# Kernel optimization log

Measured on AMD Instinct MI355X. Metric: run time of the kernel, lower is better.

Reference implementation:

```python
import jax, jax.numpy as jnp
import numpy as np

EPS = 1e-8

def rmsnorm(x, w):
    norm = jax.lax.rsqrt(jnp.mean(x * x, axis=-1, keepdims=True) + EPS)
    return x * norm * w

def setup_inputs() -> dict:
    key = jax.random.key(0)
    ks = jax.random.split(key, 10)
    B, L, D, S = 8, 4096, 1024, 256
    sD = 1.0 / np.sqrt(D)
    sS = 1.0 / np.sqrt(S)
    return {
        "x": jax.random.normal(ks[0], (B, L, D), jnp.float32),
        "w_norm": jnp.ones((D,), jnp.float32),
        "W_in": jax.random.normal(ks[1], (D, 3 * S), jnp.float32) * sD,
        "b_in": jnp.zeros((3 * S,), jnp.float32),
        "W_x": jax.random.normal(ks[2], (S, S), jnp.float32) * sS,
        "b_x": jnp.zeros((S,), jnp.float32),
        "W_dt": jax.random.normal(ks[3], (S, S), jnp.float32) * sS,
        "b_dt": jnp.zeros((S,), jnp.float32),
        "W_out": jax.random.normal(ks[4], (S, D), jnp.float32) * sS,
        "b_out": jnp.zeros((D,), jnp.float32),
    }

def reference(x, w_norm, W_in, b_in, W_x, b_x, W_dt, b_dt, W_out, b_out):
    # MambaLikeBlock forward (dropout=0 / eval mode)
    residual = x
    xn = rmsnorm(x, w_norm)
    uzg = xn @ W_in + b_in                       # [B,L,3S]
    S = uzg.shape[-1] // 3
    u, z, g = uzg[..., :S], uzg[..., S:2 * S], uzg[..., 2 * S:]
    # per-step projections are time-independent -> precompute for all t
    ut = jnp.tanh(u @ W_x + b_x)                 # [B,L,S]
    dt = jax.nn.sigmoid(z @ W_dt + b_dt)         # [B,L,S]

    def step(h, inp):
        u_t, dt_t = inp
        h = (1.0 - dt_t) * h + dt_t * u_t
        return h, h

    h0 = jnp.zeros(ut.shape[::2][::-1][:0] + (ut.shape[0], ut.shape[2]), ut.dtype)  # [B,S]
    _, hs = jax.lax.scan(step, h0, (ut.transpose(1, 0, 2), dt.transpose(1, 0, 2)))
    hs = hs.transpose(1, 0, 2)                   # [B,L,S]
    y = hs * jax.nn.sigmoid(g)
    y = y @ W_out + b_out                        # [B,L,D]
    return residual + y
```

## Files before the change

### kernel.cpp

```cpp
#include <hip/hip_runtime.h>
#include <hip/hip_bf16.h>

#define BB 8
#define LL 4096
#define DD 1024
#define SS 256
#define NTOK (BB * LL)
#define CCH 64
#define TCH (LL / CCH)

typedef short bf16x8 __attribute__((ext_vector_type(8)));
typedef float f32x4 __attribute__((ext_vector_type(4)));

__device__ __forceinline__ float bfu(unsigned short v) {
  union { unsigned int i; float f; } x;
  x.i = ((unsigned int)v) << 16;
  return x.f;
}

__device__ __forceinline__ void gl_lds16(const __hip_bfloat16* g, void* l) {
  __builtin_amdgcn_global_load_lds(
      (const __attribute__((address_space(1))) unsigned int*)g,
      (__attribute__((address_space(3))) unsigned int*)l, 16, 0, 0);
}

__global__ __launch_bounds__(256) void prep_rms(const float* __restrict__ x,
                                                const float* __restrict__ wn,
                                                __hip_bfloat16* __restrict__ xn) {
  const size_t row = blockIdx.x;
  const int t = threadIdx.x;
  const float4 xv = reinterpret_cast<const float4*>(x + row * DD)[t];
  const float4 wv = reinterpret_cast<const float4*>(wn)[t];
  float ss = xv.x * xv.x + xv.y * xv.y + xv.z * xv.z + xv.w * xv.w;
#pragma unroll
  for (int m = 32; m >= 1; m >>= 1) ss += __shfl_xor(ss, m);
  __shared__ float red[4];
  if ((t & 63) == 0) red[t >> 6] = ss;
  __syncthreads();
  const float tot = red[0] + red[1] + red[2] + red[3];
  const float r = rsqrtf(tot * (1.0f / DD) + 1e-8f);
  union { ushort4 u; __hip_bfloat16 h[4]; } o;
  o.h[0] = __float2bfloat16(xv.x * wv.x * r);
  o.h[1] = __float2bfloat16(xv.y * wv.y * r);
  o.h[2] = __float2bfloat16(xv.z * wv.z * r);
  o.h[3] = __float2bfloat16(xv.w * wv.w * r);
  reinterpret_cast<ushort4*>(xn + row * DD)[t] = o.u;
}

__global__ __launch_bounds__(256) void convT4(
    const float* __restrict__ W0, const float* __restrict__ W1,
    const float* __restrict__ W2, const float* __restrict__ W3,
    __hip_bfloat16* __restrict__ T0, __hip_bfloat16* __restrict__ T1,
    __hip_bfloat16* __restrict__ T2, __hip_bfloat16* __restrict__ T3) {
  const int seg = blockIdx.y;
  const int K = (seg == 0) ? DD : SS;
  const int Nw = (seg == 0) ? 768 : (seg == 3) ? DD : SS;
  const float* W = (seg == 0) ? W0 : (seg == 1) ? W1 : (seg == 2) ? W2 : W3;
  __hip_bfloat16* T = (seg == 0) ? T0 : (seg == 1) ? T1 : (seg == 2) ? T2 : T3;
  const int idx = blockIdx.x * 256 + threadIdx.x;
  if (idx >= K * Nw) return;
  const int k = idx / Nw, n = idx % Nw;
  T[(size_t)n * K + k] = __float2bfloat16(W[idx]);
}

template <int EPI>
__global__ __launch_bounds__(256, 2) void gemm_bf16(
    const __hip_bfloat16* __restrict__ A, int lda,
    const __hip_bfloat16* __restrict__ BT,
    const float* __restrict__ bias,
    void* __restrict__ Cptr, int ldc,
    const float* __restrict__ resid,
    int K) {
  __shared__ __align__(16) char ldsA[2][128 * 128];
  __shared__ __align__(16) char ldsB[2][128 * 128];

  const int t = threadIdx.x;
  const int bm = blockIdx.x, bn = blockIdx.y;
  const int wave = t >> 6, lane = t & 63;
  const int wr = (wave >> 1) * 64;
  const int wc = (wave & 1) * 64;
  const int lr = lane & 15;
  const int kg = lane >> 4;
  const int rsw = lr & 7;

  const int srow = lane >> 3;
  const int sg = (lane & 7) ^ srow;
  const int g_row = wave * 32 + srow;
  const __hip_bfloat16* Ab = A + (size_t)(bm * 128 + g_row) * lda + sg * 8;
  const __hip_bfloat16* Bb = BT + (size_t)(bn * 128 + g_row) * K + sg * 8;

  f32x4 acc[4][4] = {};

#define STAGE(d, koff)                                                        \
  {                                                                           \
    _Pragma("unroll") for (int p = 0; p < 4; ++p) {                           \
      gl_lds16(Ab + (size_t)(p * 8) * lda + (koff),                           \
               ldsA[d] + (wave * 32 + p * 8) * 128);                          \
      gl_lds16(Bb + (size_t)(p * 8) * K + (koff),                             \
               ldsB[d] + (wave * 32 + p * 8) * 128);                          \
    }                                                                         \
  }

  const int NT = K >> 6;
  STAGE(0, 0);

  for (int ti = 0; ti < NT; ++ti) {
    const int cur = ti & 1;
    if (ti + 1 < NT) {
      STAGE(cur ^ 1, (ti + 1) * 64);
      asm volatile("s_waitcnt vmcnt(8)" ::: "memory");
    } else {
      asm volatile("s_waitcnt vmcnt(0)" ::: "memory");
    }
    __builtin_amdgcn_sched_barrier(0);
    __builtin_amdgcn_s_barrier();
#pragma unroll
    for (int kh = 0; kh < 2; ++kh) {
      bf16x8 af[4], bfr[4];
#pragma unroll
      for (int m = 0; m < 4; ++m) {
        const int row = wr + m * 16 + lr;
        const int slot = (kg + kh * 4) ^ rsw;
        af[m] = *reinterpret_cast<const bf16x8*>(ldsA[cur] + row * 128 + slot * 16);
      }
#pragma unroll
      for (int n = 0; n < 4; ++n) {
        const int row = wc + n * 16 + lr;
        const int slot = (kg + kh * 4) ^ rsw;
        bfr[n] = *reinterpret_cast<const bf16x8*>(ldsB[cur] + row * 128 + slot * 16);
      }
#pragma unroll
      for (int m = 0; m < 4; ++m)
#pragma unroll
        for (int n = 0; n < 4; ++n)
          acc[m][n] = __builtin_amdgcn_mfma_f32_16x16x32_bf16(bfr[n], af[m],
                                                              acc[m][n], 0, 0, 0);
    }
    __builtin_amdgcn_sched_barrier(0);
    __builtin_amdgcn_s_barrier();
  }
#undef STAGE

  const int row0 = bm * 128 + wr + lr;
  const int col0 = bn * 128 + wc + kg * 4;
#pragma unroll
  for (int m = 0; m < 4; ++m) {
    const int row = row0 + m * 16;
#pragma unroll
    for (int n = 0; n < 4; ++n) {
      const int colb = col0 + n * 16;
      const float4 bv = *reinterpret_cast<const float4*>(&bias[colb]);
      float v0 = acc[m][n][0] + bv.x;
      float v1 = acc[m][n][1] + bv.y;
      float v2 = acc[m][n][2] + bv.z;
      float v3 = acc[m][n][3] + bv.w;
      if (EPI == 3) {
        const size_t off = (size_t)row * ldc + colb;
        const float4 rv = *reinterpret_cast<const float4*>(&resid[off]);
        float4 ov;
        ov.x = v0 + rv.x; ov.y = v1 + rv.y; ov.z = v2 + rv.z; ov.w = v3 + rv.w;
        *reinterpret_cast<float4*>(&((float*)Cptr)[off]) = ov;
      } else {
        if (EPI == 1) {
          v0 = tanhf(v0); v1 = tanhf(v1); v2 = tanhf(v2); v3 = tanhf(v3);
        } else if (EPI == 2) {
          v0 = 1.f / (1.f + expf(-v0)); v1 = 1.f / (1.f + expf(-v1));
          v2 = 1.f / (1.f + expf(-v2)); v3 = 1.f / (1.f + expf(-v3));
        }
        union { ushort4 u; __hip_bfloat16 h[4]; } o;
        o.h[0] = __float2bfloat16(v0); o.h[1] = __float2bfloat16(v1);
        o.h[2] = __float2bfloat16(v2); o.h[3] = __float2bfloat16(v3);
        *reinterpret_cast<ushort4*>(
            &((__hip_bfloat16*)Cptr)[(size_t)row * ldc + colb]) = o.u;
      }
    }
  }
}

__global__ __launch_bounds__(128) void scan_phase_a(
    const __hip_bfloat16* __restrict__ ut,
    const __hip_bfloat16* __restrict__ dtb,
    float* __restrict__ h0s, float* __restrict__ As) {
  const int bc = blockIdx.x;
  const int b = bc / CCH, c = bc % CCH;
  const int ch = threadIdx.x * 2;
  const size_t base = ((size_t)b * LL + (size_t)c * TCH) * SS + ch;
  float h0 = 0.f, h1 = 0.f, A0 = 1.f, A1 = 1.f;
#pragma unroll 8
  for (int t = 0; t < TCH; ++t) {
    const ushort2 uu = *reinterpret_cast<const ushort2*>(ut + base + (size_t)t * SS);
    const ushort2 dd = *reinterpret_cast<const ushort2*>(dtb + base + (size_t)t * SS);
    const float d0 = bfu(dd.x), d1 = bfu(dd.y);
    h0 = fmaf(d0, bfu(uu.x) - h0, h0);
    h1 = fmaf(d1, bfu(uu.y) - h1, h1);
    A0 *= (1.f - d0);
    A1 *= (1.f - d1);
  }
  const size_t o = (size_t)bc * SS + ch;
  *reinterpret_cast<float2*>(h0s + o) = make_float2(h0, h1);
  *reinterpret_cast<float2*>(As + o) = make_float2(A0, A1);
}

__global__ __launch_bounds__(256) void scan_phase_b(
    const float* __restrict__ h0s, const float* __restrict__ As,
    float* __restrict__ hins) {
  const int b = blockIdx.x;
  const int s = threadIdx.x;
  float hin = 0.f;
#pragma unroll 8
  for (int c = 0; c < CCH; ++c) {
    const size_t idx = ((size_t)b * CCH + c) * SS + s;
    hins[idx] = hin;
    hin = fmaf(As[idx], hin, h0s[idx]);
  }
}

__global__ __launch_bounds__(128) void scan_phase_c(
    const __hip_bfloat16* __restrict__ ut,
    const __hip_bfloat16* __restrict__ dtb,
    const __hip_bfloat16* __restrict__ gz,
    const float* __restrict__ hins,
    __hip_bfloat16* __restrict__ hsg) {
  const int bc = blockIdx.x;
  const int b = bc / CCH, c = bc % CCH;
  const int ch = threadIdx.x * 2;
  const size_t rowbase = (size_t)b * LL + (size_t)c * TCH;
  const float2 hv = *reinterpret_cast<const float2*>(hins + (size_t)bc * SS + ch);
  float h0 = hv.x, h1 = hv.y;
#pragma unroll 8
  for (int t = 0; t < TCH; ++t) {
    const size_t row = rowbase + t;
    const ushort2 uu = *reinterpret_cast<const ushort2*>(ut + row * SS + ch);
    const ushort2 dd = *reinterpret_cast<const ushort2*>(dtb + row * SS + ch);
    const ushort2 gg = *reinterpret_cast<const ushort2*>(gz + row * 768 + ch);
    h0 = fmaf(bfu(dd.x), bfu(uu.x) - h0, h0);
    h1 = fmaf(bfu(dd.y), bfu(uu.y) - h1, h1);
    union { ushort2 u; __hip_bfloat16 h[2]; } o;
    o.h[0] = __float2bfloat16(h0 / (1.f + expf(-bfu(gg.x))));
    o.h[1] = __float2bfloat16(h1 / (1.f + expf(-bfu(gg.y))));
    *reinterpret_cast<ushort2*>(hsg + row * SS + ch) = o.u;
  }
}

extern "C" void kernel_launch(void* const* d_in, const int* in_sizes, int n_in,
                              void* d_out, int out_size, void* d_ws, size_t ws_size,
                              hipStream_t stream) {
  const float* x      = (const float*)d_in[0];
  const float* w_norm = (const float*)d_in[1];
  const float* W_in   = (const float*)d_in[2];
  const float* b_in   = (const float*)d_in[3];
  const float* W_x    = (const float*)d_in[4];
  const float* b_x    = (const float*)d_in[5];
  const float* W_dt   = (const float*)d_in[6];
  const float* b_dt   = (const float*)d_in[7];
  const float* W_out  = (const float*)d_in[8];
  const float* b_out  = (const float*)d_in[9];
  float* out = (float*)d_out;

  char* w = (char*)d_ws;
  __hip_bfloat16* xn  = (__hip_bfloat16*)w;
  __hip_bfloat16* ut  = (__hip_bfloat16*)w;
  __hip_bfloat16* dtb = (__hip_bfloat16*)(w + (size_t)NTOK * SS * 2);
  w += (size_t)NTOK * DD * 2;
  __hip_bfloat16* uzg = (__hip_bfloat16*)w;  w += (size_t)NTOK * 768 * 2;
  __hip_bfloat16* WinT  = (__hip_bfloat16*)w;  w += (size_t)768 * DD * 2;
  __hip_bfloat16* WxT   = (__hip_bfloat16*)w;  w += (size_t)SS * SS * 2;
  __hip_bfloat16* WdtT  = (__hip_bfloat16*)w;  w += (size_t)SS * SS * 2;
  __hip_bfloat16* WoutT = (__hip_bfloat16*)w;  w += (size_t)DD * SS * 2;
  float* h0s  = (float*)w;  w += (size_t)BB * CCH * SS * 4;
  float* As   = (float*)w;  w += (size_t)BB * CCH * SS * 4;
  float* hins = (float*)w;  w += (size_t)BB * CCH * SS * 4;
  (void)ws_size; (void)n_in; (void)in_sizes; (void)out_size;

  convT4<<<dim3((DD * 768 + 255) / 256, 4), 256, 0, stream>>>(
      W_in, W_x, W_dt, W_out, WinT, WxT, WdtT, WoutT);

  prep_rms<<<NTOK, 256, 0, stream>>>(x, w_norm, xn);

  gemm_bf16<0><<<dim3(NTOK / 128, 768 / 128), 256, 0, stream>>>(
      xn, DD, WinT, b_in, uzg, 768, nullptr, DD);

  gemm_bf16<1><<<dim3(NTOK / 128, SS / 128), 256, 0, stream>>>(
      uzg, 768, WxT, b_x, ut, SS, nullptr, SS);
  gemm_bf16<2><<<dim3(NTOK / 128, SS / 128), 256, 0, stream>>>(
      uzg + SS, 768, WdtT, b_dt, dtb, SS, nullptr, SS);

  scan_phase_a<<<BB * CCH, 128, 0, stream>>>(ut, dtb, h0s, As);
  scan_phase_b<<<BB, 256, 0, stream>>>(h0s, As, hins);
  scan_phase_c<<<BB * CCH, 128, 0, stream>>>(ut, dtb, uzg + 2 * SS, hins, ut);

  gemm_bf16<3><<<dim3(NTOK / 128, DD / 128), 256, 0, stream>>>(
      ut, SS, WoutT, b_out, out, DD, x, SS);
}
```

Measured before the change: 276.9 us.

## Add LDS-free direct-load GEMM for K=256 projections and output GEMM

Adds a gemm_k256 kernel for the K=256 GEMMs (W_x, W_dt, W_out). It loads A and B fragments straight from global memory into registers for the MFMAs, with no LDS staging or barriers. The output GEMM gives each block two 128-column tiles so the A rows are reused across them. The old generic GEMM epilogue is reduced to a plain bf16 store, since only EPI 0 still uses it. The cost removed is LDS traffic and barrier sync on these short-K GEMMs; the trade-off is uncoalesced, non-pipelined global loads and more memory latency exposed per wave.

```diff
diff --git a/kernel.cpp b/kernel.cpp
--- a/kernel.cpp
+++ b/kernel.cpp
@@ -154,24 +154,87 @@
       float v1 = acc[m][n][1] + bv.y;
       float v2 = acc[m][n][2] + bv.z;
       float v3 = acc[m][n][3] + bv.w;
-      if (EPI == 3) {
-        const size_t off = (size_t)row * ldc + colb;
-        const float4 rv = *reinterpret_cast<const float4*>(&resid[off]);
-        float4 ov;
-        ov.x = v0 + rv.x; ov.y = v1 + rv.y; ov.z = v2 + rv.z; ov.w = v3 + rv.w;
-        *reinterpret_cast<float4*>(&((float*)Cptr)[off]) = ov;
-      } else {
-        if (EPI == 1) {
-          v0 = tanhf(v0); v1 = tanhf(v1); v2 = tanhf(v2); v3 = tanhf(v3);
-        } else if (EPI == 2) {
-          v0 = 1.f / (1.f + expf(-v0)); v1 = 1.f / (1.f + expf(-v1));
-          v2 = 1.f / (1.f + expf(-v2)); v3 = 1.f / (1.f + expf(-v3));
+      union { ushort4 u; __hip_bfloat16 h[4]; } o;
+      o.h[0] = __float2bfloat16(v0); o.h[1] = __float2bfloat16(v1);
+      o.h[2] = __float2bfloat16(v2); o.h[3] = __float2bfloat16(v3);
+      *reinterpret_cast<ushort4*>(
+          &((__hip_bfloat16*)Cptr)[(size_t)row * ldc + colb]) = o.u;
+    }
+  }
+}
+
+template <int EPI, int NBN>
+__global__ __launch_bounds__(256, 4) void gemm_k256(
+    const __hip_bfloat16* __restrict__ A, int lda,
+    const __hip_bfloat16* __restrict__ BT,
+    const float* __restrict__ bias,
+    void* __restrict__ Cptr, int ldc,
+    const float* __restrict__ resid) {
+  const int t = threadIdx.x;
+  const int bm = blockIdx.x;
+  const int wave = t >> 6, lane = t & 63;
+  const int wr = (wave >> 1) * 64;
+  const int wc = (wave & 1) * 64;
+  const int lr = lane & 15;
+  const int kg = lane >> 4;
+
+  const __hip_bfloat16* Abase =
+      A + (size_t)(bm * 128 + wr + lr) * lda + kg * 8;
+
+#pragma unroll
+  for (int bn = 0; bn < NBN; ++bn) {
+    const int ncol = (blockIdx.y * NBN + bn) * 128 + wc;
+    f32x4 acc[4][4] = {};
+#pragma unroll
+    for (int s = 0; s < 8; ++s) {
+      bf16x8 af[4], bfr[4];
+#pragma unroll
+      for (int m = 0; m < 4; ++m)
+        af[m] = *reinterpret_cast<const bf16x8*>(
+            Abase + (size_t)(m * 16) * lda + s * 32);
+#pragma unroll
+      for (int n = 0; n < 4; ++n)
+        bfr[n] = *reinterpret_cast<const bf16x8*>(
+            BT + (size_t)(ncol + n * 16 + lr) * 256 + s * 32 + kg * 8);
+#pragma unroll
+      for (int m = 0; m < 4; ++m)
+#pragma unroll
+        for (int n = 0; n < 4; ++n)
+          acc[m][n] = __builtin_amdgcn_mfma_f32_16x16x32_bf16(bfr[n], af[m],
+                                                              acc[m][n], 0, 0, 0);
+    }
+    const int row0 = bm * 128 + wr + lr;
+    const int col0 = ncol + kg * 4;
+#pragma unroll
+    for (int m = 0; m < 4; ++m) {
+      const int row = row0 + m * 16;
+#pragma unroll
+      for (int n = 0; n < 4; ++n) {
+        const int colb = col0 + n * 16;
+        const float4 bv = *reinterpret_cast<const float4*>(&bias[colb]);
+        float v0 = acc[m][n][0] + bv.x;
+        float v1 = acc[m][n][1] + bv.y;
+        float v2 = acc[m][n][2] + bv.z;
+        float v3 = acc[m][n][3] + bv.w;
+        if (EPI == 3) {
+          const size_t off = (size_t)row * ldc + colb;
+          const float4 rv = *reinterpret_cast<const float4*>(&resid[off]);
+          float4 ov;
+          ov.x = v0 + rv.x; ov.y = v1 + rv.y; ov.z = v2 + rv.z; ov.w = v3 + rv.w;
+          *reinterpret_cast<float4*>(&((float*)Cptr)[off]) = ov;
+        } else {
+          if (EPI == 1) {
+            v0 = tanhf(v0); v1 = tanhf(v1); v2 = tanhf(v2); v3 = tanhf(v3);
+          } else if (EPI == 2) {
+            v0 = 1.f / (1.f + expf(-v0)); v1 = 1.f / (1.f + expf(-v1));
+            v2 = 1.f / (1.f + expf(-v2)); v3 = 1.f / (1.f + expf(-v3));
+          }
+          union { ushort4 u; __hip_bfloat16 h[4]; } o;
+          o.h[0] = __float2bfloat16(v0); o.h[1] = __float2bfloat16(v1);
+          o.h[2] = __float2bfloat16(v2); o.h[3] = __float2bfloat16(v3);
+          *reinterpret_cast<ushort4*>(
+              &((__hip_bfloat16*)Cptr)[(size_t)row * ldc + colb]) = o.u;
         }
-        union { ushort4 u; __hip_bfloat16 h[4]; } o;
-        o.h[0] = __float2bfloat16(v0); o.h[1] = __float2bfloat16(v1);
-        o.h[2] = __float2bfloat16(v2); o.h[3] = __float2bfloat16(v3);
-        *reinterpret_cast<ushort4*>(
-            &((__hip_bfloat16*)Cptr)[(size_t)row * ldc + colb]) = o.u;
       }
     }
   }
@@ -280,15 +343,15 @@
   gemm_bf16<0><<<dim3(NTOK / 128, 768 / 128), 256, 0, stream>>>(
       xn, DD, WinT, b_in, uzg, 768, nullptr, DD);
 
-  gemm_bf16<1><<<dim3(NTOK / 128, SS / 128), 256, 0, stream>>>(
-      uzg, 768, WxT, b_x, ut, SS, nullptr, SS);
-  gemm_bf16<2><<<dim3(NTOK / 128, SS / 128), 256, 0, stream>>>(
-      uzg + SS, 768, WdtT, b_dt, dtb, SS, nullptr, SS);
+  gemm_k256<1, 1><<<dim3(NTOK / 128, 2), 256, 0, stream>>>(
+      uzg, 768, WxT, b_x, ut, SS, nullptr);
+  gemm_k256<2, 1><<<dim3(NTOK / 128, 2), 256, 0, stream>>>(
+      uzg + SS, 768, WdtT, b_dt, dtb, SS, nullptr);
 
   scan_phase_a<<<BB * CCH, 128, 0, stream>>>(ut, dtb, h0s, As);
   scan_phase_b<<<BB, 256, 0, stream>>>(h0s, As, hins);
   scan_phase_c<<<BB * CCH, 128, 0, stream>>>(ut, dtb, uzg + 2 * SS, hins, ut);
 
-  gemm_bf16<3><<<dim3(NTOK / 128, DD / 128), 256, 0, stream>>>(
-      ut, SS, WoutT, b_out, out, DD, x, SS);
-}
+  gemm_k256<3, 2><<<dim3(NTOK / 128, 4), 256, 0, stream>>>(
+      ut, SS, WoutT, b_out, out, DD, x);
+}
```

Measured after the change: 375.1 us. 1.35x slower.
